# Kernel optimization log

Hardware: AMD Instinct MI355X
Metric: run time of the kernel (lower is better)

The kernel has to match this reference:

```python
import jax, jax.numpy as jnp
import numpy as np
from jax import lax

B = 32
NUM_CLASSES = 80
NUM_ANCHORS = 3
IMG_SIZE = 320
STRIDES = (8, 16, 32)
TOPK = 1000
CONF_THRESH = 0.05
NMS_THRESH = 0.6
EPS = 1e-10

ANCHOR_SIZES = np.array([[16, 16], [32, 32], [64, 48],
                         [64, 64], [96, 96], [128, 96],
                         [128, 128], [192, 160], [256, 256]],
                        dtype=np.float32).reshape(3, NUM_ANCHORS, 2)


def _build_anchors():
    # mirrors YOWOv3.generate_anchors
    boxes, strides = [], []
    for lvl, s in enumerate(STRIDES):
        f = IMG_SIZE // s
        ys, xs = np.meshgrid(np.arange(f), np.arange(f), indexing='ij')
        xy = np.stack([xs, ys], axis=-1).astype(np.float32).reshape(-1, 1, 2)
        xy = np.repeat(xy, NUM_ANCHORS, axis=1) * s            # [f*f, A, 2]
        wh = np.broadcast_to(ANCHOR_SIZES[lvl], (f * f, NUM_ANCHORS, 2))
        boxes.append(np.concatenate([xy, wh], axis=-1).reshape(-1, 4))
        strides.append(np.full(f * f * NUM_ANCHORS, s, dtype=np.float32))
    return np.concatenate(boxes, 0), np.concatenate(strides, 0)


def setup_inputs() -> dict:
    key = jax.random.key(0)
    k1, k2, k3 = jax.random.split(key, 3)
    anchors_np, stride_np = _build_anchors()
    M = anchors_np.shape[0]  # 6300
    conf_pred = jax.random.normal(k1, (B, M, 1), dtype=jnp.float32)
    cls_pred = jax.random.normal(k2, (B, M, NUM_CLASSES), dtype=jnp.float32) * 2.0
    reg_pred = jax.random.normal(k3, (B, M, 4), dtype=jnp.float32) * 0.5
    return {
        'conf_pred': conf_pred,
        'cls_pred': cls_pred,
        'reg_pred': reg_pred,
        'anchors': jnp.asarray(anchors_np),
        'stride_map': jnp.asarray(stride_np),
    }


def _decode_boxes(anchors, stride_map, reg_pred):
    # anchors [M,4] (cx, cy, w, h) in pixels; reg_pred [B,M,4]
    ctr = anchors[None, :, :2] + jax.nn.sigmoid(reg_pred[..., :2]) * stride_map[None, :, None]
    wh = anchors[None, :, 2:] * jnp.exp(reg_pred[..., 2:])
    return jnp.concatenate([ctr - 0.5 * wh, ctr + 0.5 * wh], axis=-1)  # [B,M,4] x1y1x2y2


def _nms_keep(boxes, scores, labels):
    # boxes [K,4] sorted by descending score; per-class greedy NMS -> bool keep [K]
    x1, y1, x2, y2 = boxes[:, 0], boxes[:, 1], boxes[:, 2], boxes[:, 3]
    areas = (x2 - x1) * (y2 - y1)
    xx1 = jnp.maximum(x1[:, None], x1[None, :])
    yy1 = jnp.maximum(y1[:, None], y1[None, :])
    xx2 = jnp.minimum(x2[:, None], x2[None, :])
    yy2 = jnp.minimum(y2[:, None], y2[None, :])
    inter = jnp.maximum(EPS, xx2 - xx1) * jnp.maximum(EPS, yy2 - yy1)
    union = jnp.maximum(areas[:, None] + areas[None, :] - inter, EPS)
    iou = inter / union
    suppress = (iou > NMS_THRESH) & (labels[:, None] == labels[None, :])
    keep0 = scores >= CONF_THRESH
    idxs = jnp.arange(boxes.shape[0])

    def body(i, keep):
        # if box i is kept, suppress all later same-class boxes with iou > thresh
        return keep & ~(keep[i] & suppress[i] & (idxs > i))

    return lax.fori_loop(0, boxes.shape[0], body, keep0)


def reference(conf_pred, cls_pred, reg_pred, anchors, stride_map):
    box_pred = _decode_boxes(anchors, stride_map, reg_pred)              # [B,M,4]
    joint = jax.nn.sigmoid(conf_pred) * jax.nn.softmax(cls_pred, -1)     # [B,M,C]
    scores = jnp.max(joint, axis=-1)                                     # [B,M]
    labels = jnp.argmax(joint, axis=-1)                                  # [B,M]

    top_scores, top_idx = lax.top_k(scores, TOPK)                        # sorted desc
    top_labels = jnp.take_along_axis(labels, top_idx, axis=1)
    top_boxes = jnp.take_along_axis(box_pred, top_idx[..., None], axis=1)
    top_boxes = jnp.clip(top_boxes / IMG_SIZE, 0.0, 1.0)                 # [B,K,4]

    keep = jax.vmap(_nms_keep)(top_boxes, top_scores, top_labels)        # [B,K] bool
    return top_scores, top_labels, top_boxes, keep
```

## Files before the change

kernel.cpp:

```cpp
#include <hip/hip_runtime.h>
#include <stdint.h>

#define NB 32
#define NM 6300
#define NC 80
#define NTOP 1000
#define NPAD 1024
#define NCAND 2048
#define NBINS 4096

static constexpr float IMGSZ   = 320.0f;
static constexpr float CONF_TH = 0.05f;
static constexpr float NMS_TH  = 0.6f;
static constexpr float EPSF    = 1e-10f;

static constexpr size_t OFF_SCORES = 0;
static constexpr size_t OFF_LABELS = OFF_SCORES + (size_t)NB * NM * 4;
static constexpr size_t OFF_TIDX   = OFF_LABELS + (size_t)NB * NM * 4;
static constexpr size_t OFF_NBOX   = OFF_TIDX   + (size_t)NB * NPAD * 4;
static constexpr size_t OFF_NLAB   = OFF_NBOX   + (size_t)NB * NPAD * 16;
static constexpr size_t OFF_SUP    = ((OFF_NLAB + (size_t)NB * NPAD * 4) + 1023) & ~(size_t)1023;

__global__ __launch_bounds__(256) void k_score(const float* __restrict__ conf,
                                               const float* __restrict__ cls,
                                               float* __restrict__ scores,
                                               int* __restrict__ labels) {
#pragma clang fp contract(off)
    int t = blockIdx.x * blockDim.x + threadIdx.x;
    int a = t >> 4;
    int l = t & 15;
    if (a >= NB * NM) return;
    const float* row = cls + (size_t)a * NC;

    float v[5];
#pragma unroll
    for (int k = 0; k < 5; ++k) v[k] = row[l + 16 * k];

    float bv = v[0];
    int bi = l;
#pragma unroll
    for (int k = 1; k < 5; ++k) {
        int c = l + 16 * k;
        if (v[k] > bv) { bv = v[k]; bi = c; }
    }
#pragma unroll
    for (int m = 1; m < 16; m <<= 1) {
        float ov = __shfl_xor(bv, m, 16);
        int   oi = __shfl_xor(bi, m, 16);
        if (ov > bv || (ov == bv && oi < bi)) { bv = ov; bi = oi; }
    }
    float s = 0.0f;
#pragma unroll
    for (int k = 0; k < 5; ++k) s += expf(v[k] - bv);
#pragma unroll
    for (int m = 1; m < 16; m <<= 1) s += __shfl_xor(s, m, 16);

    if (l == 0) {
        float cf  = conf[a];
        float sig = 1.0f / (1.0f + expf(-cf));
        float inv = 1.0f / s;
        scores[a] = sig * inv;
        labels[a] = bi;
    }
}

__global__ __launch_bounds__(1024) void k_topk(const float* __restrict__ scores,
                                               float* __restrict__ out_scores,
                                               int* __restrict__ top_idx) {
    __shared__ uint32_t hist[NBINS];
    __shared__ __align__(16) uint64_t key[NCAND];
    __shared__ int sT, scnt;
    int b = blockIdx.x, tid = threadIdx.x;
    const float* sb = scores + (size_t)b * NM;

    for (int i = tid; i < NBINS; i += 1024) hist[i] = 0;
    for (int i = tid; i < NCAND; i += 1024) key[i] = 0;
    if (tid == 0) scnt = 0;
    __syncthreads();

    for (int i = tid; i < NM; i += 1024)
        atomicAdd(&hist[__float_as_uint(sb[i]) >> 20], 1u);
    __syncthreads();

    if (tid < 64) {
        int l = tid;
        uint32_t q = 0;
        for (int k = 0; k < 64; ++k) q += hist[l * 64 + ((k + l) & 63)];
        uint32_t s = q;
        for (int off = 1; off < 64; off <<= 1) {
            uint32_t o = __shfl_down(s, off);
            if (l + off < 64) s += o;
        }
        uint64_t m = __ballot(s >= (uint32_t)NTOP);
        int c = 63 - __clzll(m);
        uint32_t sc_ = __shfl(s, c);
        uint32_t qc  = __shfl(q, c);
        uint32_t tail = sc_ - qc;
        uint32_t v = hist[c * 64 + l];
        uint32_t s2 = v;
        for (int off = 1; off < 64; off <<= 1) {
            uint32_t o = __shfl_down(s2, off);
            if (l + off < 64) s2 += o;
        }
        uint64_t m2 = __ballot(s2 + tail >= (uint32_t)NTOP);
        int T = c * 64 + (63 - __clzll(m2));
        if (l == 0) sT = T;
    }
    __syncthreads();

    uint32_t T = (uint32_t)sT;
    int lane = tid & 63;
    for (int i = tid; i < NM; i += 1024) {
        uint32_t bits = __float_as_uint(sb[i]);
        bool pred = (bits >> 20) >= T;
        uint64_t mask = __ballot(pred);
        if (pred) {
            int leader = __ffsll((unsigned long long)mask) - 1;
            int prefix = __popcll(mask & ((1ull << lane) - 1));
            int base = 0;
            if (lane == leader) base = atomicAdd(&scnt, (int)__popcll(mask));
            base = __shfl(base, leader);
            int pos = base + prefix;
            if (pos < NCAND)
                key[pos] = ((uint64_t)bits << 32) | (uint32_t)(~(uint32_t)i);
        }
    }
    __syncthreads();

    int C = scnt; if (C > NCAND) C = NCAND;
    int C2 = (C + 1) >> 1;
    int jmax = (C2 + 3) & ~3;
    const ulonglong2* k2 = (const ulonglong2*)key;
    for (int t = tid; t < C; t += 1024) {
        uint64_t kt = key[t];
        uint32_t rank = 0;
        for (int j = 0; j < jmax; j += 4) {
            ulonglong2 a0 = k2[j + 0];
            ulonglong2 a1 = k2[j + 1];
            ulonglong2 a2 = k2[j + 2];
            ulonglong2 a3 = k2[j + 3];
            rank += (a0.x > kt) ? 1u : 0u;
            rank += (a0.y > kt) ? 1u : 0u;
            rank += (a1.x > kt) ? 1u : 0u;
            rank += (a1.y > kt) ? 1u : 0u;
            rank += (a2.x > kt) ? 1u : 0u;
            rank += (a2.y > kt) ? 1u : 0u;
            rank += (a3.x > kt) ? 1u : 0u;
            rank += (a3.y > kt) ? 1u : 0u;
        }
        if (rank < (uint32_t)NTOP) {
            out_scores[b * NTOP + rank] = __uint_as_float((uint32_t)(kt >> 32));
            top_idx[b * NPAD + rank]    = (int)(~(uint32_t)kt);
        }
    }
}

__global__ __launch_bounds__(256) void k_decode(const int* __restrict__ top_idx,
                                                const int* __restrict__ labels,
                                                const float* __restrict__ reg,
                                                const float* __restrict__ anchors,
                                                const float* __restrict__ stridemap,
                                                float* __restrict__ out_labels,
                                                float* __restrict__ out_boxes,
                                                float* __restrict__ nbox,
                                                int* __restrict__ nlab) {
#pragma clang fp contract(off)
    int t = blockIdx.x * blockDim.x + threadIdx.x;
    if (t >= NB * NTOP) return;
    int b = t / NTOP, r = t % NTOP;
    int idx = top_idx[b * NPAD + r];
    int lab = labels[(size_t)b * NM + idx];
    out_labels[b * NTOP + r] = (float)lab;

    const float* rg = reg + ((size_t)b * NM + idx) * 4;
    float rx = rg[0], ry = rg[1], rw = rg[2], rh = rg[3];
    const float* an = anchors + (size_t)idx * 4;
    float ax = an[0], ay = an[1], aw = an[2], ah = an[3];
    float st = stridemap[idx];

    float sx = 1.0f / (1.0f + expf(-rx));
    float sy = 1.0f / (1.0f + expf(-ry));
    float cx = ax + sx * st;
    float cy = ay + sy * st;
    float w  = aw * expf(rw);
    float h  = ah * expf(rh);
    float x1 = cx - 0.5f * w, y1 = cy - 0.5f * h;
    float x2 = cx + 0.5f * w, y2 = cy + 0.5f * h;

    float nx1 = fminf(fmaxf(x1 / IMGSZ, 0.0f), 1.0f);
    float ny1 = fminf(fmaxf(y1 / IMGSZ, 0.0f), 1.0f);
    float nx2 = fminf(fmaxf(x2 / IMGSZ, 0.0f), 1.0f);
    float ny2 = fminf(fmaxf(y2 / IMGSZ, 0.0f), 1.0f);

    float4 bx = make_float4(nx1, ny1, nx2, ny2);
    ((float4*)out_boxes)[b * NTOP + r] = bx;
    ((float4*)nbox)[b * NPAD + r]      = bx;
    nlab[b * NPAD + r] = lab;
}

__global__ __launch_bounds__(256) void k_supmat(const float* __restrict__ nbox,
                                                const int* __restrict__ nlab,
                                                uint64_t* __restrict__ sup) {
#pragma clang fp contract(off)
    int b = blockIdx.y;
    int t = blockIdx.x;
    int tj = (int)((sqrtf(8.0f * (float)t + 1.0f) - 1.0f) * 0.5f);
    while ((tj + 1) * (tj + 2) / 2 <= t) ++tj;
    while (tj * (tj + 1) / 2 > t) --tj;
    int ti = t - tj * (tj + 1) / 2;

    int lane = threadIdx.x & 63;
    int w    = threadIdx.x >> 6;

    int i = ti * 64 + lane;
    int j = tj * 64 + lane;

    float4 bi = ((const float4*)nbox)[b * NPAD + i];
    float  ai = (bi.z - bi.x) * (bi.w - bi.y);
    int    li = nlab[b * NPAD + i];
    float4 bj = ((const float4*)nbox)[b * NPAD + j];
    int    lj = nlab[b * NPAD + j];
    bool   iv = (i < NTOP);

    uint64_t mybits = 0;
#pragma unroll
    for (int u = 0; u < 16; ++u) {
        int jj = (w << 4) | u;
        float bjx = __shfl(bj.x, jj);
        float bjy = __shfl(bj.y, jj);
        float bjz = __shfl(bj.z, jj);
        float bjw = __shfl(bj.w, jj);
        int   ljv = __shfl(lj, jj);
        float ajv = (bjz - bjx) * (bjw - bjy);
        int   jg  = tj * 64 + jj;
        float xx1 = fmaxf(bi.x, bjx);
        float yy1 = fmaxf(bi.y, bjy);
        float xx2 = fminf(bi.z, bjz);
        float yy2 = fminf(bi.w, bjw);
        float inter = fmaxf(EPSF, xx2 - xx1) * fmaxf(EPSF, yy2 - yy1);
        float uni   = fmaxf(ai + ajv - inter, EPSF);
        float iou   = inter / uni;
        bool pred = (i < jg) && iv && (jg < NTOP) && (li == ljv) && (iou > NMS_TH);
        uint64_t bal = __ballot(pred);
        if (lane == jj) mybits = bal;
    }
    if ((lane >> 4) == w)
        sup[(((size_t)b * 16 + tj) * 16 + ti) * 64 + lane] = mybits;
}

__global__ __launch_bounds__(1024) void k_nms(const float* __restrict__ out_scores,
                                              const uint64_t* __restrict__ sup,
                                              float* __restrict__ out_keep) {
    __shared__ uint64_t Kw[16];
    int b    = blockIdx.x;
    int w    = threadIdx.x >> 6;
    int lane = threadIdx.x & 63;
    const uint64_t* supb = sup + (size_t)b * 16 * 16 * 64;

    uint64_t wrow[16];
#pragma unroll
    for (int ti = 0; ti < 16; ++ti)
        wrow[ti] = (ti <= w) ? supb[((size_t)w * 16 + ti) * 64 + lane] : 0ULL;

    int pos = w * 64 + lane;
    bool k0 = (pos < NTOP) && (out_scores[b * NTOP + pos] >= CONF_TH);

    uint64_t ext = 0;
#pragma unroll
    for (int s = 0; s < 16; ++s) {
        if (w == s) {
            bool cand = k0 && (ext == 0ULL);
            uint64_t wself = wrow[s];
            uint64_t alive = __ballot(cand);
            for (int it = 0; it < 64; ++it) {
                bool dead = (wself & alive) != 0ULL;
                uint64_t na = __ballot(cand && !dead);
                if (na == alive) break;
                alive = na;
            }
            if (lane == 0) Kw[s] = alive;
            if (pos < NTOP)
                out_keep[b * NTOP + pos] = ((alive >> lane) & 1ULL) ? 1.0f : 0.0f;
        }
        __syncthreads();
        if (w > s) ext |= wrow[s] & Kw[s];
    }
}

extern "C" void kernel_launch(void* const* d_in, const int* in_sizes, int n_in,
                              void* d_out, int out_size, void* d_ws, size_t ws_size,
                              hipStream_t stream) {
    const float* conf = (const float*)d_in[0];
    const float* cls  = (const float*)d_in[1];
    const float* reg  = (const float*)d_in[2];
    const float* anch = (const float*)d_in[3];
    const float* strm = (const float*)d_in[4];

    float* out        = (float*)d_out;
    float* out_scores = out;
    float* out_labels = out + NB * NTOP;
    float* out_boxes  = out + 2 * NB * NTOP;
    float* out_keep   = out + 2 * NB * NTOP + NB * NTOP * 4;

    char* ws = (char*)d_ws;
    float*    scores = (float*)(ws + OFF_SCORES);
    int*      labels = (int*)(ws + OFF_LABELS);
    int*      tidx   = (int*)(ws + OFF_TIDX);
    float*    nbox   = (float*)(ws + OFF_NBOX);
    int*      nlab   = (int*)(ws + OFF_NLAB);
    uint64_t* sup    = (uint64_t*)(ws + OFF_SUP);

    k_score<<<(NB * NM * 16) / 256, 256, 0, stream>>>(conf, cls, scores, labels);
    k_topk<<<NB, 1024, 0, stream>>>(scores, out_scores, tidx);
    k_decode<<<(NB * NTOP + 255) / 256, 256, 0, stream>>>(tidx, labels, reg, anch, strm,
                                                          out_labels, out_boxes, nbox, nlab);
    k_supmat<<<dim3(136, NB), 256, 0, stream>>>(nbox, nlab, sup);
    k_nms<<<NB, 1024, 0, stream>>>(out_scores, sup, out_keep);
}
```

Measured before the change: 79.29 us.

## Split per-batch top-k into multi-block histogram, compact and rank-decode kernels

The single-block-per-batch top-k kernel becomes several kernels. The histogram is now built with global atomics inside the scoring kernel, a small kernel picks the threshold bin, an 8-slice-per-batch kernel compacts candidates into global memory, and a multi-block rank kernel ranks candidates and fuses the box decode. The aim is to replace 32 serial 1024-thread blocks with more parallel work and to drop the separate decode pass. In exchange it adds a zeroing kernel, more launches and global-memory atomic contention.

```diff
diff --git a/kernel.cpp b/kernel.cpp
--- a/kernel.cpp
+++ b/kernel.cpp
@@ -8,6 +8,8 @@
 #define NPAD 1024
 #define NCAND 2048
 #define NBINS 4096
+#define NSLICE 8
+#define SLICE 800
 
 static constexpr float IMGSZ   = 320.0f;
 static constexpr float CONF_TH = 0.05f;
@@ -16,15 +18,26 @@
 
 static constexpr size_t OFF_SCORES = 0;
 static constexpr size_t OFF_LABELS = OFF_SCORES + (size_t)NB * NM * 4;
-static constexpr size_t OFF_TIDX   = OFF_LABELS + (size_t)NB * NM * 4;
-static constexpr size_t OFF_NBOX   = OFF_TIDX   + (size_t)NB * NPAD * 4;
+static constexpr size_t OFF_HIST   = OFF_LABELS + (size_t)NB * NM * 4;
+static constexpr size_t OFF_CNT    = OFF_HIST   + (size_t)NB * NBINS * 4;
+static constexpr size_t OFF_TB     = OFF_CNT    + (size_t)NB * 4;
+static constexpr size_t OFF_CAND   = OFF_TB     + (size_t)NB * 4;
+static constexpr size_t OFF_NBOX   = OFF_CAND   + (size_t)NB * NCAND * 8;
 static constexpr size_t OFF_NLAB   = OFF_NBOX   + (size_t)NB * NPAD * 16;
 static constexpr size_t OFF_SUP    = ((OFF_NLAB + (size_t)NB * NPAD * 4) + 1023) & ~(size_t)1023;
+
+__global__ __launch_bounds__(256) void k_zero(uint32_t* __restrict__ hist,
+                                              int* __restrict__ cnt) {
+    int t = blockIdx.x * 256 + threadIdx.x;
+    if (t < NB * NBINS) hist[t] = 0;
+    if (t < NB) cnt[t] = 0;
+}
 
 __global__ __launch_bounds__(256) void k_score(const float* __restrict__ conf,
                                                const float* __restrict__ cls,
                                                float* __restrict__ scores,
-                                               int* __restrict__ labels) {
+                                               int* __restrict__ labels,
+                                               uint32_t* __restrict__ hist) {
 #pragma clang fp contract(off)
     int t = blockIdx.x * blockDim.x + threadIdx.x;
     int a = t >> 4;
@@ -59,58 +72,63 @@
         float cf  = conf[a];
         float sig = 1.0f / (1.0f + expf(-cf));
         float inv = 1.0f / s;
-        scores[a] = sig * inv;
+        float sc  = sig * inv;
+        scores[a] = sc;
         labels[a] = bi;
-    }
-}
-
-__global__ __launch_bounds__(1024) void k_topk(const float* __restrict__ scores,
-                                               float* __restrict__ out_scores,
-                                               int* __restrict__ top_idx) {
-    __shared__ uint32_t hist[NBINS];
-    __shared__ __align__(16) uint64_t key[NCAND];
-    __shared__ int sT, scnt;
-    int b = blockIdx.x, tid = threadIdx.x;
+        int bb = a / NM;
+        atomicAdd(&hist[(size_t)bb * NBINS + (__float_as_uint(sc) >> 20)], 1u);
+    }
+}
+
+__global__ __launch_bounds__(64) void k_thresh(const uint32_t* __restrict__ hist,
+                                               int* __restrict__ Tb) {
+    int b = blockIdx.x;
+    int l = threadIdx.x;
+    const uint4* h4 = (const uint4*)(hist + (size_t)b * NBINS + l * 64);
+
+    uint32_t q = 0;
+#pragma unroll
+    for (int k = 0; k < 16; k += 4) {
+        uint4 a0 = h4[k + 0], a1 = h4[k + 1], a2 = h4[k + 2], a3 = h4[k + 3];
+        q += a0.x + a0.y + a0.z + a0.w;
+        q += a1.x + a1.y + a1.z + a1.w;
+        q += a2.x + a2.y + a2.z + a2.w;
+        q += a3.x + a3.y + a3.z + a3.w;
+    }
+    uint32_t s = q;
+    for (int off = 1; off < 64; off <<= 1) {
+        uint32_t o = __shfl_down(s, off);
+        if (l + off < 64) s += o;
+    }
+    uint64_t m = __ballot(s >= (uint32_t)NTOP);
+    int c = 63 - __clzll(m);
+    uint32_t sc_ = __shfl(s, c);
+    uint32_t qc  = __shfl(q, c);
+    uint32_t tail = sc_ - qc;
+    uint32_t v = hist[(size_t)b * NBINS + c * 64 + l];
+    uint32_t s2 = v;
+    for (int off = 1; off < 64; off <<= 1) {
+        uint32_t o = __shfl_down(s2, off);
+        if (l + off < 64) s2 += o;
+    }
+    uint64_t m2 = __ballot(s2 + tail >= (uint32_t)NTOP);
+    int T = c * 64 + (63 - __clzll(m2));
+    if (l == 0) Tb[b] = T;
+}
+
+__global__ __launch_bounds__(256) void k_compact(const float* __restrict__ scores,
+                                                 const int* __restrict__ Tb,
+                                                 uint64_t* __restrict__ cand,
+                                                 int* __restrict__ cnt) {
+    int b = blockIdx.y;
+    int sl = blockIdx.x;
+    uint32_t T = (uint32_t)Tb[b];
     const float* sb = scores + (size_t)b * NM;
-
-    for (int i = tid; i < NBINS; i += 1024) hist[i] = 0;
-    for (int i = tid; i < NCAND; i += 1024) key[i] = 0;
-    if (tid == 0) scnt = 0;
-    __syncthreads();
-
-    for (int i = tid; i < NM; i += 1024)
-        atomicAdd(&hist[__float_as_uint(sb[i]) >> 20], 1u);
-    __syncthreads();
-
-    if (tid < 64) {
-        int l = tid;
-        uint32_t q = 0;
-        for (int k = 0; k < 64; ++k) q += hist[l * 64 + ((k + l) & 63)];
-        uint32_t s = q;
-        for (int off = 1; off < 64; off <<= 1) {
-            uint32_t o = __shfl_down(s, off);
-            if (l + off < 64) s += o;
-        }
-        uint64_t m = __ballot(s >= (uint32_t)NTOP);
-        int c = 63 - __clzll(m);
-        uint32_t sc_ = __shfl(s, c);
-        uint32_t qc  = __shfl(q, c);
-        uint32_t tail = sc_ - qc;
-        uint32_t v = hist[c * 64 + l];
-        uint32_t s2 = v;
-        for (int off = 1; off < 64; off <<= 1) {
-            uint32_t o = __shfl_down(s2, off);
-            if (l + off < 64) s2 += o;
-        }
-        uint64_t m2 = __ballot(s2 + tail >= (uint32_t)NTOP);
-        int T = c * 64 + (63 - __clzll(m2));
-        if (l == 0) sT = T;
-    }
-    __syncthreads();
-
-    uint32_t T = (uint32_t)sT;
-    int lane = tid & 63;
-    for (int i = tid; i < NM; i += 1024) {
+    int lo = sl * SLICE;
+    int hi = lo + SLICE; if (hi > NM) hi = NM;
+    int lane = threadIdx.x & 63;
+
+    for (int i = lo + threadIdx.x; i < hi; i += 256) {
         uint32_t bits = __float_as_uint(sb[i]);
         bool pred = (bits >> 20) >= T;
         uint64_t mask = __ballot(pred);
@@ -118,59 +136,60 @@
             int leader = __ffsll((unsigned long long)mask) - 1;
             int prefix = __popcll(mask & ((1ull << lane) - 1));
             int base = 0;
-            if (lane == leader) base = atomicAdd(&scnt, (int)__popcll(mask));
+            if (lane == leader) base = atomicAdd(&cnt[b], (int)__popcll(mask));
             base = __shfl(base, leader);
             int pos = base + prefix;
             if (pos < NCAND)
-                key[pos] = ((uint64_t)bits << 32) | (uint32_t)(~(uint32_t)i);
+                cand[(size_t)b * NCAND + pos] =
+                    ((uint64_t)bits << 32) | (uint32_t)(~(uint32_t)i);
         }
     }
+}
+
+__global__ __launch_bounds__(256) void k_rank(const uint64_t* __restrict__ cand,
+                                              const int* __restrict__ cnt,
+                                              const int* __restrict__ labels,
+                                              const float* __restrict__ reg,
+                                              const float* __restrict__ anchors,
+                                              const float* __restrict__ stridemap,
+                                              float* __restrict__ out_scores,
+                                              float* __restrict__ out_labels,
+                                              float* __restrict__ out_boxes,
+                                              float* __restrict__ nbox,
+                                              int* __restrict__ nlab) {
+#pragma clang fp contract(off)
+    __shared__ __align__(16) uint64_t key[NCAND];
+    int b    = blockIdx.y;
+    int tpos = blockIdx.x * 256 + threadIdx.x;
+    int C = cnt[b]; if (C > NCAND) C = NCAND;
+    int Cr = (C + 7) & ~7;
+
+    for (int i = threadIdx.x; i < Cr; i += 256)
+        key[i] = (i < C) ? cand[(size_t)b * NCAND + i] : 0ULL;
     __syncthreads();
 
-    int C = scnt; if (C > NCAND) C = NCAND;
-    int C2 = (C + 1) >> 1;
-    int jmax = (C2 + 3) & ~3;
-    const ulonglong2* k2 = (const ulonglong2*)key;
-    for (int t = tid; t < C; t += 1024) {
-        uint64_t kt = key[t];
-        uint32_t rank = 0;
-        for (int j = 0; j < jmax; j += 4) {
-            ulonglong2 a0 = k2[j + 0];
-            ulonglong2 a1 = k2[j + 1];
-            ulonglong2 a2 = k2[j + 2];
-            ulonglong2 a3 = k2[j + 3];
-            rank += (a0.x > kt) ? 1u : 0u;
-            rank += (a0.y > kt) ? 1u : 0u;
-            rank += (a1.x > kt) ? 1u : 0u;
-            rank += (a1.y > kt) ? 1u : 0u;
-            rank += (a2.x > kt) ? 1u : 0u;
-            rank += (a2.y > kt) ? 1u : 0u;
-            rank += (a3.x > kt) ? 1u : 0u;
-            rank += (a3.y > kt) ? 1u : 0u;
-        }
-        if (rank < (uint32_t)NTOP) {
-            out_scores[b * NTOP + rank] = __uint_as_float((uint32_t)(kt >> 32));
-            top_idx[b * NPAD + rank]    = (int)(~(uint32_t)kt);
-        }
-    }
-}
-
-__global__ __launch_bounds__(256) void k_decode(const int* __restrict__ top_idx,
-                                                const int* __restrict__ labels,
-                                                const float* __restrict__ reg,
-                                                const float* __restrict__ anchors,
-                                                const float* __restrict__ stridemap,
-                                                float* __restrict__ out_labels,
-                                                float* __restrict__ out_boxes,
-                                                float* __restrict__ nbox,
-                                                int* __restrict__ nlab) {
-#pragma clang fp contract(off)
-    int t = blockIdx.x * blockDim.x + threadIdx.x;
-    if (t >= NB * NTOP) return;
-    int b = t / NTOP, r = t % NTOP;
-    int idx = top_idx[b * NPAD + r];
+    if (tpos >= C) return;
+    uint64_t kt = key[tpos];
+    uint32_t rank = 0;
+    for (int j = 0; j < Cr; j += 8) {
+        const ulonglong2* k2 = (const ulonglong2*)(key + j);
+        ulonglong2 a0 = k2[0], a1 = k2[1], a2 = k2[2], a3 = k2[3];
+        rank += (a0.x > kt) ? 1u : 0u;
+        rank += (a0.y > kt) ? 1u : 0u;
+        rank += (a1.x > kt) ? 1u : 0u;
+        rank += (a1.y > kt) ? 1u : 0u;
+        rank += (a2.x > kt) ? 1u : 0u;
+        rank += (a2.y > kt) ? 1u : 0u;
+        rank += (a3.x > kt) ? 1u : 0u;
+        rank += (a3.y > kt) ? 1u : 0u;
+    }
+    if (rank >= (uint32_t)NTOP) return;
+
+    uint32_t sbits = (uint32_t)(kt >> 32);
+    int idx = (int)(~(uint32_t)kt);
+    out_scores[b * NTOP + rank] = __uint_as_float(sbits);
     int lab = labels[(size_t)b * NM + idx];
-    out_labels[b * NTOP + r] = (float)lab;
+    out_labels[b * NTOP + rank] = (float)lab;
 
     const float* rg = reg + ((size_t)b * NM + idx) * 4;
     float rx = rg[0], ry = rg[1], rw = rg[2], rh = rg[3];
@@ -193,9 +212,9 @@
     float ny2 = fminf(fmaxf(y2 / IMGSZ, 0.0f), 1.0f);
 
     float4 bx = make_float4(nx1, ny1, nx2, ny2);
-    ((float4*)out_boxes)[b * NTOP + r] = bx;
-    ((float4*)nbox)[b * NPAD + r]      = bx;
-    nlab[b * NPAD + r] = lab;
+    ((float4*)out_boxes)[b * NTOP + rank] = bx;
+    ((float4*)nbox)[b * NPAD + rank]      = bx;
+    nlab[b * NPAD + rank] = lab;
 }
 
 __global__ __launch_bounds__(256) void k_supmat(const float* __restrict__ nbox,
@@ -305,15 +324,21 @@
     char* ws = (char*)d_ws;
     float*    scores = (float*)(ws + OFF_SCORES);
     int*      labels = (int*)(ws + OFF_LABELS);
-    int*      tidx   = (int*)(ws + OFF_TIDX);
+    uint32_t* hist   = (uint32_t*)(ws + OFF_HIST);
+    int*      cnt    = (int*)(ws + OFF_CNT);
+    int*      Tb     = (int*)(ws + OFF_TB);
+    uint64_t* cand   = (uint64_t*)(ws + OFF_CAND);
     float*    nbox   = (float*)(ws + OFF_NBOX);
     int*      nlab   = (int*)(ws + OFF_NLAB);
     uint64_t* sup    = (uint64_t*)(ws + OFF_SUP);
 
-    k_score<<<(NB * NM * 16) / 256, 256, 0, stream>>>(conf, cls, scores, labels);
-    k_topk<<<NB, 1024, 0, stream>>>(scores, out_scores, tidx);
-    k_decode<<<(NB * NTOP + 255) / 256, 256, 0, stream>>>(tidx, labels, reg, anch, strm,
-                                                          out_labels, out_boxes, nbox, nlab);
+    k_zero<<<(NB * NBINS + 255) / 256, 256, 0, stream>>>(hist, cnt);
+    k_score<<<(NB * NM * 16) / 256, 256, 0, stream>>>(conf, cls, scores, labels, hist);
+    k_thresh<<<NB, 64, 0, stream>>>(hist, Tb);
+    k_compact<<<dim3(NSLICE, NB), 256, 0, stream>>>(scores, Tb, cand, cnt);
+    k_rank<<<dim3(NCAND / 256, NB), 256, 0, stream>>>(cand, cnt, labels, reg, anch, strm,
+                                                      out_scores, out_labels, out_boxes,
+                                                      nbox, nlab);
     k_supmat<<<dim3(136, NB), 256, 0, stream>>>(nbox, nlab, sup);
     k_nms<<<NB, 1024, 0, stream>>>(out_scores, sup, out_keep);
 }
```

New measurement: 135.9 us. +71.4%, slower.
